# Kernel optimization log

Measured on AMD Instinct MI355X. Metric: run time of the kernel, lower is better.

Reference implementation:

```python
import jax, jax.numpy as jnp
import numpy as np

SHRINKAGE = 0.1  # matches init_kwargs shrinkage_rate


def setup_inputs() -> dict:
    key = jax.random.key(0)
    k0, k1, k2, k3 = jax.random.split(key, 4)
    B, F, T, D, P = 8192, 256, 32, 6, 8
    N = 2 ** D - 1  # internal nodes per tree
    L = 2 ** D      # leaves per tree
    return {
        "x": jax.random.normal(k0, (B, F), dtype=jnp.float32),
        "W": jax.random.normal(k1, (T, N, F), dtype=jnp.float32) / np.float32(np.sqrt(F)),
        "b": jax.random.normal(k2, (T, N), dtype=jnp.float32) * 0.01,
        "phi": jax.random.normal(k3, (T, L, P), dtype=jnp.float32),
    }


def reference(x, W, b, phi):
    # x: [B,F]; W: [T,N,F]; b: [T,N]; phi: [T,L,P]
    T, N, F = W.shape
    L = N + 1
    D = int(round(np.log2(L)))
    # all node gating probabilities in one batched GEMM: p(right) per internal node
    s = jax.nn.sigmoid(jnp.einsum('bf,tnf->btn', x, W) + b)  # [B,T,N]
    # heap (level-order) node indexing: node at level d with prefix q has index 2^d-1+q;
    # leaf l's bit at level d is (l >> (D-1-d)) & 1 (1 -> right child -> prob s, 0 -> 1-s)
    leaves = np.arange(L)
    leaf_prob = jnp.ones(s.shape[:2] + (L,), dtype=s.dtype)  # [B,T,L]
    for d in range(D):  # static small loop over tree depth
        bits = jnp.asarray((leaves >> (D - 1 - d)) & 1, dtype=bool)
        idx = (2 ** d - 1) + (leaves >> (D - d))
        sd = s[:, :, idx]  # [B,T,L]
        leaf_prob = leaf_prob * jnp.where(bits, sd, 1.0 - sd)
    # per-tree prediction = sum_l path_prob_l * phi_l; GBM output = shrinkage * sum_t
    tree_pred = jnp.einsum('btl,tlp->btp', leaf_prob, phi)  # [B,T,P]
    return SHRINKAGE * tree_pred.sum(axis=1)  # [B,P]
```

## Files before the change

kernel.cpp:

```cpp
#include <hip/hip_runtime.h>

#define B_TOT   8192
#define F_DIM   256
#define T_TREES 32
#define N_NODES 63
#define P_DIM   8
#define BM      128
#define SHRINK  0.1f

typedef __bf16 bf16_t;
typedef bf16_t bf16x8 __attribute__((ext_vector_type(8)));
typedef bf16_t bf16x2 __attribute__((ext_vector_type(2)));
typedef float  f32x4  __attribute__((ext_vector_type(4)));
typedef float  f32x2  __attribute__((ext_vector_type(2)));
typedef unsigned short ushort8_t __attribute__((ext_vector_type(8)));
typedef unsigned short ushort4_t __attribute__((ext_vector_type(4)));

__device__ __forceinline__ unsigned short f2bf(float f) {
    unsigned int u = __float_as_uint(f);
    u += 0x7fffu + ((u >> 16) & 1u);
    return (unsigned short)(u >> 16);
}
__device__ __forceinline__ unsigned short f2bf_hw(float f) {
    const __bf16 b = (__bf16)f;
    return __builtin_bit_cast(unsigned short, b);
}
__device__ __forceinline__ unsigned int pk2bf_hw(float a, float b) {
    f32x2 v; v.x = a; v.y = b;
    const bf16x2 r = __builtin_convertvector(v, bf16x2);
    return __builtin_bit_cast(unsigned int, r);
}
__device__ __forceinline__ float fast_rcp(float x) {
#if __has_builtin(__builtin_amdgcn_rcpf)
    return __builtin_amdgcn_rcpf(x);
#else
    return 1.0f / x;
#endif
}
__device__ __forceinline__ void gl_lds16(const void* g, void* l) {
    __builtin_amdgcn_global_load_lds(
        (const __attribute__((address_space(1))) unsigned int*)g,
        (__attribute__((address_space(3))) unsigned int*)l, 16, 0, 0);
}

__global__ __launch_bounds__(256) void cvt_all(
    const float* __restrict__ x, const float* __restrict__ W,
    const float* __restrict__ phi,
    unsigned short* __restrict__ xb, unsigned short* __restrict__ Wb,
    unsigned short* __restrict__ phiB, float* __restrict__ out)
{
    const int bx  = blockIdx.x;
    const int tid = threadIdx.x;
    if (bx < 2048) {
        const int i = bx * 256 + tid;
        const float4 v = *(const float4*)&x[(size_t)i * 4];
        ushort4_t h;
        h.x = f2bf(v.x); h.y = f2bf(v.y); h.z = f2bf(v.z); h.w = f2bf(v.w);
        *(ushort4_t*)&xb[(size_t)i * 4] = h;
    } else if (bx < 2560) {
        const int i = (bx - 2048) * 256 + tid;
        const int tree = i >> 12;
        const int rem  = i & 4095;
        const int row  = rem >> 6;
        const int c4   = rem & 63;
        float4 v = make_float4(0.f, 0.f, 0.f, 0.f);
        if (row < N_NODES)
            v = *(const float4*)&W[((size_t)(tree * N_NODES + row)) * F_DIM + c4 * 4];
        ushort4_t h;
        h.x = f2bf(v.x); h.y = f2bf(v.y); h.z = f2bf(v.z); h.w = f2bf(v.w);
        *(ushort4_t*)&Wb[(size_t)i * 4] = h;
    } else if (bx < 2576) {
        const int i = (bx - 2560) * 256 + tid;
        const int tree = i >> 7;
        const int rem  = i & 127;
        const int k2   = rem >> 6;
        const int lane = rem & 63;
        const int lm   = lane & 15;
        const int quad = lane >> 4;
        ushort8_t h;
#pragma unroll
        for (int j = 0; j < 8; ++j) {
            float v = 0.f;
            if (lm < 8) v = phi[(size_t)tree * 512 + (k2 * 32 + quad * 8 + j) * 8 + lm];
            h[j] = f2bf(v);
        }
        *(ushort8_t*)&phiB[(size_t)i * 8] = h;
    } else {
        const int i = (bx - 2576) * 256 + tid;
        *(float4*)&out[(size_t)i * 4] = make_float4(0.f, 0.f, 0.f, 0.f);
    }
}

__global__ __launch_bounds__(256, 4) void softgbm_main(
    const unsigned short* __restrict__ xb, const unsigned short* __restrict__ Wb,
    const unsigned short* __restrict__ phiB, const float* __restrict__ bias,
    float* __restrict__ out)
{
    __shared__ union Smem {
        struct { unsigned short A[BM * 64]; unsigned short B[BM * 64]; } g;
        unsigned short ss[2 * BM * 64];
    } sm;
    __shared__ float bs2[2][64];

    const int tid  = threadIdx.x;
    const int tp   = blockIdx.x;
    const int b0   = blockIdx.y * BM;
    const int wave = tid >> 6;
    const int lane = tid & 63;
    const int quad = lane >> 4;
    const int lm   = lane & 15;
    const int wr   = wave >> 1;
    const int wc   = wave & 1;

    if (tid < 128) {
        const int p = tid >> 6, node = tid & 63;
        bs2[p][node] = (node < N_NODES) ? bias[(tp * 2 + p) * N_NODES + node] : 0.f;
    }

    f32x4 acc[4][4];
#pragma unroll
    for (int m = 0; m < 4; ++m)
#pragma unroll
        for (int n = 0; n < 4; ++n)
            acc[m][n] = f32x4{0.f, 0.f, 0.f, 0.f};

    for (int ko = 0; ko < F_DIM; ko += 64) {
        __syncthreads();
#pragma unroll
        for (int i = 0; i < 4; ++i) {
            const int r = wave * 32 + i * 8 + (lane >> 3);
            const int c = (lane & 7) ^ (r & 7);
            gl_lds16(&xb[(size_t)(b0 + r) * F_DIM + ko + c * 8],
                     &sm.g.A[(wave * 32 + i * 8) * 64]);
        }
#pragma unroll
        for (int i = 0; i < 4; ++i) {
            const int r = wave * 32 + i * 8 + (lane >> 3);
            const int c = (lane & 7) ^ (r & 7);
            gl_lds16(&Wb[(size_t)(tp * 128 + r) * F_DIM + ko + c * 8],
                     &sm.g.B[(wave * 32 + i * 8) * 64]);
        }
        __syncthreads();

#pragma unroll
        for (int ks = 0; ks < 2; ++ks) {
            bf16x8 af[4], bfr[4];
#pragma unroll
            for (int m = 0; m < 4; ++m) {
                const int r  = wr * 64 + m * 16 + lm;
                const int cp = (ks * 4 + quad) ^ (r & 7);
                af[m] = __builtin_bit_cast(bf16x8, *(ushort8_t*)&sm.g.A[r * 64 + cp * 8]);
            }
#pragma unroll
            for (int n = 0; n < 4; ++n) {
                const int r  = wc * 64 + n * 16 + lm;
                const int cp = (ks * 4 + quad) ^ (r & 7);
                bfr[n] = __builtin_bit_cast(bf16x8, *(ushort8_t*)&sm.g.B[r * 64 + cp * 8]);
            }
#pragma unroll
            for (int m = 0; m < 4; ++m)
#pragma unroll
                for (int n = 0; n < 4; ++n)
                    acc[m][n] = __builtin_amdgcn_mfma_f32_16x16x32_bf16(af[m], bfr[n], acc[m][n], 0, 0, 0);
        }
    }
    __syncthreads();

    bf16x8 pb[2][2];
#pragma unroll
    for (int p = 0; p < 2; ++p)
#pragma unroll
        for (int k2 = 0; k2 < 2; ++k2)
            pb[p][k2] = __builtin_bit_cast(bf16x8,
                *(const ushort8_t*)&phiB[(size_t)(((tp * 2 + p) * 2 + k2) * 64 + lane) * 8]);

    int slot[4];
#pragma unroll
    for (int n = 0; n < 4; ++n) {
        const int node = n * 16 + lm;
        const int np1  = node + 1;
        const int d    = 31 - __builtin_clz(np1);
        if (d == 0) slot[n] = 0;
        else {
            const int half = 1 << (d - 1);
            const int u    = np1 - (1 << d);
            const int hh   = (u >= half) ? 1 : 0;
            const int pos  = half + (u & (half - 1));
            slot[n] = hh * 32 + pos;
        }
    }

#pragma unroll
    for (int m = 0; m < 4; ++m)
#pragma unroll
        for (int n = 0; n < 4; ++n) {
            const int node = n * 16 + lm;
            const float bb = bs2[wc][node];
#pragma unroll
            for (int reg = 0; reg < 4; ++reg) {
                const int rr = wr * 64 + m * 16 + quad * 4 + reg;
                const float z = acc[m][n][reg] + bb;
                const float e = __expf(-z);
                const unsigned short sv = f2bf_hw(fast_rcp(1.0f + e));
                if (node < N_NODES) {
                    unsigned short* base = &sm.ss[(wc * BM + rr) * 64];
                    base[slot[n]] = sv;
                    if (node == 0) base[32] = sv;
                }
            }
        }
    __syncthreads();

    const int row = tid >> 1;
    const int h   = tid & 1;
    const int rs  = row & 7;

    f32x4 accp[2] = { f32x4{0.f,0.f,0.f,0.f}, f32x4{0.f,0.f,0.f,0.f} };

    for (int p = 0; p < 2; ++p) {
        unsigned short* ssp = &sm.ss[p * (BM * 64)];
        unsigned int w[16];
        {
            const unsigned short* sp = &ssp[row * 64 + h * 32];
            *(uint4*)&w[0]  = *(const uint4*)&sp[0];
            *(uint4*)&w[4]  = *(const uint4*)&sp[8];
            *(uint4*)&w[8]  = *(const uint4*)&sp[16];
            *(uint4*)&w[12] = *(const uint4*)&sp[24];
        }
#define VAL(j) ((j) & 1 ? __uint_as_float(w[(j) >> 1] & 0xffff0000u) \
                        : __uint_as_float(w[(j) >> 1] << 16))
        const float s0 = VAL(0);
        const float q1 = h ? s0 : (1.0f - s0);
        float q2[2], q3[4], q4[8], q5[16];
        {
            const float tv = VAL(1);
            q2[1] = q1 * tv; q2[0] = q1 - q2[1];
        }
#pragma unroll
        for (int v = 0; v < 2; ++v) {
            const float tv = VAL(2 + v);
            q3[2 * v + 1] = q2[v] * tv; q3[2 * v] = q2[v] - q3[2 * v + 1];
        }
#pragma unroll
        for (int v = 0; v < 4; ++v) {
            const float tv = VAL(4 + v);
            q4[2 * v + 1] = q3[v] * tv; q4[2 * v] = q3[v] - q4[2 * v + 1];
        }
#pragma unroll
        for (int v = 0; v < 8; ++v) {
            const float tv = VAL(8 + v);
            q5[2 * v + 1] = q4[v] * tv; q5[2 * v] = q4[v] - q5[2 * v + 1];
        }
#pragma unroll
        for (int i = 0; i < 4; ++i) {
            float q6[8];
#pragma unroll
            for (int v = 0; v < 4; ++v) {
                const float tv = VAL(16 + i * 4 + v);
                q6[2 * v + 1] = q5[i * 4 + v] * tv;
                q6[2 * v]     = q5[i * 4 + v] - q6[2 * v + 1];
            }
            uint4 wv;
            wv.x = pk2bf_hw(q6[0], q6[1]);
            wv.y = pk2bf_hw(q6[2], q6[3]);
            wv.z = pk2bf_hw(q6[4], q6[5]);
            wv.w = pk2bf_hw(q6[6], q6[7]);
            *(uint4*)&ssp[row * 64 + ((h * 4 + i) ^ rs) * 8] = wv;
        }
#undef VAL

#pragma unroll
        for (int mg = 0; mg < 2; ++mg)
#pragma unroll
            for (int k2 = 0; k2 < 2; ++k2) {
                const int r2 = wave * 32 + mg * 16 + lm;
                const int cp = (k2 * 4 + quad) ^ (r2 & 7);
                const bf16x8 afr = __builtin_bit_cast(bf16x8,
                    *(ushort8_t*)&ssp[r2 * 64 + cp * 8]);
                accp[mg] = __builtin_amdgcn_mfma_f32_16x16x32_bf16(afr, pb[p][k2], accp[mg], 0, 0, 0);
            }
    }

    if (lm < P_DIM) {
#pragma unroll
        for (int mg = 0; mg < 2; ++mg)
#pragma unroll
            for (int reg = 0; reg < 4; ++reg) {
                const int r2 = wave * 32 + mg * 16 + quad * 4 + reg;
                atomicAdd(&out[(size_t)(b0 + r2) * P_DIM + lm], SHRINK * accp[mg][reg]);
            }
    }
}

extern "C" void kernel_launch(void* const* d_in, const int* in_sizes, int n_in,
                              void* d_out, int out_size, void* d_ws, size_t ws_size,
                              hipStream_t stream) {
    const float* x    = (const float*)d_in[0];
    const float* W    = (const float*)d_in[1];
    const float* bias = (const float*)d_in[2];
    const float* phi  = (const float*)d_in[3];
    float* out = (float*)d_out;

    unsigned short* xb   = (unsigned short*)d_ws;
    unsigned short* Wb   = xb + (size_t)B_TOT * F_DIM;
    unsigned short* phiB = Wb + (size_t)T_TREES * 64 * F_DIM;

    cvt_all<<<dim3(2640), dim3(256), 0, stream>>>(x, W, phi, xb, Wb, phiB, out);

    dim3 grid(T_TREES / 2, B_TOT / BM);
    softgbm_main<<<grid, dim3(256), 0, stream>>>(xb, Wb, phiB, bias, out);
}
```

Measured before the change: 82.75 us.

## Assign one tree per block and drop cross-wave barriers in epilogue

The main kernel now processes a single tree per block instead of two, doubling the grid. Each wave owns 32 batch rows against all 64 nodes, and the launch-bounds occupancy hint rises from 4 to 5. Because each wave now writes and reads only its own rows of the shared sigmoid buffer, the two __syncthreads barriers between the GEMM, the sigmoid scatter and the leaf-probability stage are removed. The shared-memory footprint shrinks and the phi fragment loads move before the GEMM loop. In exchange, each x tile is loaded once per tree rather than once per tree pair, doubling x traffic, and the number of atomic adds into the output doubles.

```diff
diff --git a/kernel.cpp b/kernel.cpp
--- a/kernel.cpp
+++ b/kernel.cpp
@@ -91,35 +91,36 @@
     }
 }
 
-__global__ __launch_bounds__(256, 4) void softgbm_main(
+__global__ __launch_bounds__(256, 5) void softgbm_main(
     const unsigned short* __restrict__ xb, const unsigned short* __restrict__ Wb,
     const unsigned short* __restrict__ phiB, const float* __restrict__ bias,
     float* __restrict__ out)
 {
     __shared__ union Smem {
-        struct { unsigned short A[BM * 64]; unsigned short B[BM * 64]; } g;
-        unsigned short ss[2 * BM * 64];
+        struct { unsigned short A[BM * 64]; unsigned short B[64 * 64]; } g;
+        unsigned short ss[BM * 64];
     } sm;
-    __shared__ float bs2[2][64];
+    __shared__ float bs[64];
 
     const int tid  = threadIdx.x;
-    const int tp   = blockIdx.x;
+    const int t    = blockIdx.x;
     const int b0   = blockIdx.y * BM;
     const int wave = tid >> 6;
     const int lane = tid & 63;
     const int quad = lane >> 4;
     const int lm   = lane & 15;
-    const int wr   = wave >> 1;
-    const int wc   = wave & 1;
-
-    if (tid < 128) {
-        const int p = tid >> 6, node = tid & 63;
-        bs2[p][node] = (node < N_NODES) ? bias[(tp * 2 + p) * N_NODES + node] : 0.f;
-    }
-
-    f32x4 acc[4][4];
-#pragma unroll
-    for (int m = 0; m < 4; ++m)
+
+    if (tid < 64) bs[tid] = (tid < N_NODES) ? bias[t * N_NODES + tid] : 0.f;
+
+    bf16x8 pb[2];
+#pragma unroll
+    for (int k2 = 0; k2 < 2; ++k2)
+        pb[k2] = __builtin_bit_cast(bf16x8,
+            *(const ushort8_t*)&phiB[(size_t)((t * 2 + k2) * 64 + lane) * 8]);
+
+    f32x4 acc[2][4];
+#pragma unroll
+    for (int m = 0; m < 2; ++m)
 #pragma unroll
         for (int n = 0; n < 4; ++n)
             acc[m][n] = f32x4{0.f, 0.f, 0.f, 0.f};
@@ -134,45 +135,36 @@
                      &sm.g.A[(wave * 32 + i * 8) * 64]);
         }
 #pragma unroll
-        for (int i = 0; i < 4; ++i) {
-            const int r = wave * 32 + i * 8 + (lane >> 3);
+        for (int i = 0; i < 2; ++i) {
+            const int r = wave * 16 + i * 8 + (lane >> 3);
             const int c = (lane & 7) ^ (r & 7);
-            gl_lds16(&Wb[(size_t)(tp * 128 + r) * F_DIM + ko + c * 8],
-                     &sm.g.B[(wave * 32 + i * 8) * 64]);
+            gl_lds16(&Wb[(size_t)(t * 64 + r) * F_DIM + ko + c * 8],
+                     &sm.g.B[(wave * 16 + i * 8) * 64]);
         }
         __syncthreads();
 
 #pragma unroll
         for (int ks = 0; ks < 2; ++ks) {
-            bf16x8 af[4], bfr[4];
-#pragma unroll
-            for (int m = 0; m < 4; ++m) {
-                const int r  = wr * 64 + m * 16 + lm;
+            bf16x8 af[2], bfr[4];
+#pragma unroll
+            for (int m = 0; m < 2; ++m) {
+                const int r  = wave * 32 + m * 16 + lm;
                 const int cp = (ks * 4 + quad) ^ (r & 7);
                 af[m] = __builtin_bit_cast(bf16x8, *(ushort8_t*)&sm.g.A[r * 64 + cp * 8]);
             }
 #pragma unroll
             for (int n = 0; n < 4; ++n) {
-                const int r  = wc * 64 + n * 16 + lm;
+                const int r  = n * 16 + lm;
                 const int cp = (ks * 4 + quad) ^ (r & 7);
                 bfr[n] = __builtin_bit_cast(bf16x8, *(ushort8_t*)&sm.g.B[r * 64 + cp * 8]);
             }
 #pragma unroll
-            for (int m = 0; m < 4; ++m)
+            for (int m = 0; m < 2; ++m)
 #pragma unroll
                 for (int n = 0; n < 4; ++n)
                     acc[m][n] = __builtin_amdgcn_mfma_f32_16x16x32_bf16(af[m], bfr[n], acc[m][n], 0, 0, 0);
         }
     }
-    __syncthreads();
-
-    bf16x8 pb[2][2];
-#pragma unroll
-    for (int p = 0; p < 2; ++p)
-#pragma unroll
-        for (int k2 = 0; k2 < 2; ++k2)
-            pb[p][k2] = __builtin_bit_cast(bf16x8,
-                *(const ushort8_t*)&phiB[(size_t)(((tp * 2 + p) * 2 + k2) * 64 + lane) * 8]);
 
     int slot[4];
 #pragma unroll
@@ -191,95 +183,91 @@
     }
 
 #pragma unroll
-    for (int m = 0; m < 4; ++m)
+    for (int m = 0; m < 2; ++m)
 #pragma unroll
         for (int n = 0; n < 4; ++n) {
             const int node = n * 16 + lm;
-            const float bb = bs2[wc][node];
+            const float bb = bs[node];
 #pragma unroll
             for (int reg = 0; reg < 4; ++reg) {
-                const int rr = wr * 64 + m * 16 + quad * 4 + reg;
+                const int rr = wave * 32 + m * 16 + quad * 4 + reg;
                 const float z = acc[m][n][reg] + bb;
                 const float e = __expf(-z);
                 const unsigned short sv = f2bf_hw(fast_rcp(1.0f + e));
                 if (node < N_NODES) {
-                    unsigned short* base = &sm.ss[(wc * BM + rr) * 64];
+                    unsigned short* base = &sm.ss[rr * 64];
                     base[slot[n]] = sv;
                     if (node == 0) base[32] = sv;
                 }
             }
         }
-    __syncthreads();
 
     const int row = tid >> 1;
     const int h   = tid & 1;
     const int rs  = row & 7;
-
-    f32x4 accp[2] = { f32x4{0.f,0.f,0.f,0.f}, f32x4{0.f,0.f,0.f,0.f} };
-
-    for (int p = 0; p < 2; ++p) {
-        unsigned short* ssp = &sm.ss[p * (BM * 64)];
-        unsigned int w[16];
-        {
-            const unsigned short* sp = &ssp[row * 64 + h * 32];
-            *(uint4*)&w[0]  = *(const uint4*)&sp[0];
-            *(uint4*)&w[4]  = *(const uint4*)&sp[8];
-            *(uint4*)&w[8]  = *(const uint4*)&sp[16];
-            *(uint4*)&w[12] = *(const uint4*)&sp[24];
-        }
+    unsigned short* srow = &sm.ss[row * 64];
+
+    unsigned int w[16];
+    {
+        const unsigned short* sp = &srow[h * 32];
+        *(uint4*)&w[0]  = *(const uint4*)&sp[0];
+        *(uint4*)&w[4]  = *(const uint4*)&sp[8];
+        *(uint4*)&w[8]  = *(const uint4*)&sp[16];
+        *(uint4*)&w[12] = *(const uint4*)&sp[24];
+    }
 #define VAL(j) ((j) & 1 ? __uint_as_float(w[(j) >> 1] & 0xffff0000u) \
                         : __uint_as_float(w[(j) >> 1] << 16))
-        const float s0 = VAL(0);
-        const float q1 = h ? s0 : (1.0f - s0);
-        float q2[2], q3[4], q4[8], q5[16];
-        {
-            const float tv = VAL(1);
-            q2[1] = q1 * tv; q2[0] = q1 - q2[1];
-        }
-#pragma unroll
-        for (int v = 0; v < 2; ++v) {
-            const float tv = VAL(2 + v);
-            q3[2 * v + 1] = q2[v] * tv; q3[2 * v] = q2[v] - q3[2 * v + 1];
-        }
+    const float s0 = VAL(0);
+    const float q1 = h ? s0 : (1.0f - s0);
+    float q2[2], q3[4], q4[8], q5[16];
+    {
+        const float tv = VAL(1);
+        q2[1] = q1 * tv; q2[0] = q1 - q2[1];
+    }
+#pragma unroll
+    for (int v = 0; v < 2; ++v) {
+        const float tv = VAL(2 + v);
+        q3[2 * v + 1] = q2[v] * tv; q3[2 * v] = q2[v] - q3[2 * v + 1];
+    }
+#pragma unroll
+    for (int v = 0; v < 4; ++v) {
+        const float tv = VAL(4 + v);
+        q4[2 * v + 1] = q3[v] * tv; q4[2 * v] = q3[v] - q4[2 * v + 1];
+    }
+#pragma unroll
+    for (int v = 0; v < 8; ++v) {
+        const float tv = VAL(8 + v);
+        q5[2 * v + 1] = q4[v] * tv; q5[2 * v] = q4[v] - q5[2 * v + 1];
+    }
+#pragma unroll
+    for (int i = 0; i < 4; ++i) {
+        float q6[8];
 #pragma unroll
         for (int v = 0; v < 4; ++v) {
-            const float tv = VAL(4 + v);
-            q4[2 * v + 1] = q3[v] * tv; q4[2 * v] = q3[v] - q4[2 * v + 1];
-        }
-#pragma unroll
-        for (int v = 0; v < 8; ++v) {
-            const float tv = VAL(8 + v);
-            q5[2 * v + 1] = q4[v] * tv; q5[2 * v] = q4[v] - q5[2 * v + 1];
-        }
-#pragma unroll
-        for (int i = 0; i < 4; ++i) {
-            float q6[8];
-#pragma unroll
-            for (int v = 0; v < 4; ++v) {
-                const float tv = VAL(16 + i * 4 + v);
-                q6[2 * v + 1] = q5[i * 4 + v] * tv;
-                q6[2 * v]     = q5[i * 4 + v] - q6[2 * v + 1];
-            }
-            uint4 wv;
-            wv.x = pk2bf_hw(q6[0], q6[1]);
-            wv.y = pk2bf_hw(q6[2], q6[3]);
-            wv.z = pk2bf_hw(q6[4], q6[5]);
-            wv.w = pk2bf_hw(q6[6], q6[7]);
-            *(uint4*)&ssp[row * 64 + ((h * 4 + i) ^ rs) * 8] = wv;
-        }
+            const float tv = VAL(16 + i * 4 + v);
+            q6[2 * v + 1] = q5[i * 4 + v] * tv;
+            q6[2 * v]     = q5[i * 4 + v] - q6[2 * v + 1];
+        }
+        uint4 wv;
+        wv.x = pk2bf_hw(q6[0], q6[1]);
+        wv.y = pk2bf_hw(q6[2], q6[3]);
+        wv.z = pk2bf_hw(q6[4], q6[5]);
+        wv.w = pk2bf_hw(q6[6], q6[7]);
+        *(uint4*)&srow[((h * 4 + i) ^ rs) * 8] = wv;
+    }
 #undef VAL
 
-#pragma unroll
-        for (int mg = 0; mg < 2; ++mg)
-#pragma unroll
-            for (int k2 = 0; k2 < 2; ++k2) {
-                const int r2 = wave * 32 + mg * 16 + lm;
-                const int cp = (k2 * 4 + quad) ^ (r2 & 7);
-                const bf16x8 afr = __builtin_bit_cast(bf16x8,
-                    *(ushort8_t*)&ssp[r2 * 64 + cp * 8]);
-                accp[mg] = __builtin_amdgcn_mfma_f32_16x16x32_bf16(afr, pb[p][k2], accp[mg], 0, 0, 0);
-            }
-    }
+    f32x4 accp[2] = { f32x4{0.f,0.f,0.f,0.f}, f32x4{0.f,0.f,0.f,0.f} };
+#pragma unroll
+    for (int mg = 0; mg < 2; ++mg)
+#pragma unroll
+        for (int k2 = 0; k2 < 2; ++k2) {
+            const int r2 = wave * 32 + mg * 16 + lm;
+            const int cp = (k2 * 4 + quad) ^ (r2 & 7);
+            const bf16x8 afr = __builtin_bit_cast(bf16x8,
+                *(ushort8_t*)&sm.ss[r2 * 64 + cp * 8]);
+            accp[mg] = __builtin_amdgcn_mfma_f32_16x16x32_bf16(afr, pb[k2], accp[mg], 0, 0, 0);
+        }
 
     if (lm < P_DIM) {
 #pragma unroll
@@ -307,6 +295,6 @@
 
     cvt_all<<<dim3(2640), dim3(256), 0, stream>>>(x, W, phi, xb, Wb, phiB, out);
 
-    dim3 grid(T_TREES / 2, B_TOT / BM);
+    dim3 grid(T_TREES, B_TOT / BM);
     softgbm_main<<<grid, dim3(256), 0, stream>>>(xb, Wb, phiB, bias, out);
 }
```

After: 88.64 us. 1.07x slower.

## Double-buffer GEMM K-loop in LDS with 32-wide slices and prefetch

Applied to the files above, without the earlier changes.

Splits the shared-memory A/B tiles into two 32-column buffers and prefetches the next K slice via direct global-to-LDS loads while MFMAs run on the current one. The loop now has 8 iterations with one barrier each instead of 4 iterations with two barriers, and uses a new rotation-based swizzle for the narrower rows. The aim is to hide global load latency behind compute. The cost is more iterations and barriers per K element, and the new swizzle may cause LDS bank conflicts.

```diff
diff --git a/kernel.cpp b/kernel.cpp
--- a/kernel.cpp
+++ b/kernel.cpp
@@ -97,7 +97,7 @@
     float* __restrict__ out)
 {
     __shared__ union Smem {
-        struct { unsigned short A[BM * 64]; unsigned short B[BM * 64]; } g;
+        struct { unsigned short A[2][BM * 32]; unsigned short B[2][BM * 32]; } g;
         unsigned short ss[2 * BM * 64];
     } sm;
     __shared__ float bs2[2][64];
@@ -111,6 +111,8 @@
     const int lm   = lane & 15;
     const int wr   = wave >> 1;
     const int wc   = wave & 1;
+    const int sr   = lane >> 2;
+    const int pc   = lane & 3;
 
     if (tid < 128) {
         const int p = tid >> 6, node = tid & 63;
@@ -124,38 +126,47 @@
         for (int n = 0; n < 4; ++n)
             acc[m][n] = f32x4{0.f, 0.f, 0.f, 0.f};
 
-    for (int ko = 0; ko < F_DIM; ko += 64) {
-        __syncthreads();
-#pragma unroll
-        for (int i = 0; i < 4; ++i) {
-            const int r = wave * 32 + i * 8 + (lane >> 3);
-            const int c = (lane & 7) ^ (r & 7);
-            gl_lds16(&xb[(size_t)(b0 + r) * F_DIM + ko + c * 8],
-                     &sm.g.A[(wave * 32 + i * 8) * 64]);
-        }
-#pragma unroll
-        for (int i = 0; i < 4; ++i) {
-            const int r = wave * 32 + i * 8 + (lane >> 3);
-            const int c = (lane & 7) ^ (r & 7);
-            gl_lds16(&Wb[(size_t)(tp * 128 + r) * F_DIM + ko + c * 8],
-                     &sm.g.B[(wave * 32 + i * 8) * 64]);
-        }
-        __syncthreads();
-
-#pragma unroll
-        for (int ks = 0; ks < 2; ++ks) {
+
+#pragma unroll
+    for (int i = 0; i < 2; ++i) {
+        const int r  = wave * 32 + i * 16 + sr;
+        const int lc = (pc - (r >> 1)) & 3;
+        gl_lds16(&xb[(size_t)(b0 + r) * F_DIM + lc * 8],
+                 &sm.g.A[0][(wave * 32 + i * 16) * 32]);
+        gl_lds16(&Wb[(size_t)(tp * 128 + r) * F_DIM + lc * 8],
+                 &sm.g.B[0][(wave * 32 + i * 16) * 32]);
+    }
+    __syncthreads();
+
+#pragma unroll
+    for (int it = 0; it < 8; ++it) {
+        if (it < 7) {
+            const int ko  = (it + 1) * 32;
+            const int buf = (it + 1) & 1;
+#pragma unroll
+            for (int i = 0; i < 2; ++i) {
+                const int r  = wave * 32 + i * 16 + sr;
+                const int lc = (pc - (r >> 1)) & 3;
+                gl_lds16(&xb[(size_t)(b0 + r) * F_DIM + ko + lc * 8],
+                         &sm.g.A[buf][(wave * 32 + i * 16) * 32]);
+                gl_lds16(&Wb[(size_t)(tp * 128 + r) * F_DIM + ko + lc * 8],
+                         &sm.g.B[buf][(wave * 32 + i * 16) * 32]);
+            }
+        }
+        {
+            const int buf = it & 1;
             bf16x8 af[4], bfr[4];
 #pragma unroll
             for (int m = 0; m < 4; ++m) {
                 const int r  = wr * 64 + m * 16 + lm;
-                const int cp = (ks * 4 + quad) ^ (r & 7);
-                af[m] = __builtin_bit_cast(bf16x8, *(ushort8_t*)&sm.g.A[r * 64 + cp * 8]);
+                const int cp = (quad + (r >> 1)) & 3;
+                af[m] = __builtin_bit_cast(bf16x8, *(ushort8_t*)&sm.g.A[buf][r * 32 + cp * 8]);
             }
 #pragma unroll
             for (int n = 0; n < 4; ++n) {
                 const int r  = wc * 64 + n * 16 + lm;
-                const int cp = (ks * 4 + quad) ^ (r & 7);
-                bfr[n] = __builtin_bit_cast(bf16x8, *(ushort8_t*)&sm.g.B[r * 64 + cp * 8]);
+                const int cp = (quad + (r >> 1)) & 3;
+                bfr[n] = __builtin_bit_cast(bf16x8, *(ushort8_t*)&sm.g.B[buf][r * 32 + cp * 8]);
             }
 #pragma unroll
             for (int m = 0; m < 4; ++m)
@@ -163,8 +174,8 @@
                 for (int n = 0; n < 4; ++n)
                     acc[m][n] = __builtin_amdgcn_mfma_f32_16x16x32_bf16(af[m], bfr[n], acc[m][n], 0, 0, 0);
         }
-    }
-    __syncthreads();
+        __syncthreads();
+    }
 
     bf16x8 pb[2][2];
 #pragma unroll
```

New measurement: 84.52 us. 2.1% more time.
